# Kernel tuning notes

Measured on AMD Instinct MI355X. Metric: run time of the kernel, lower is better.

## Reference

```python
import jax, jax.numpy as jnp
import numpy as np

ROUTING_ITERS = 3

def squash(t, axis=-1):
    norm = jnp.linalg.norm(t, axis=axis, keepdims=True)
    scale = norm ** 2 / (1 + norm ** 2)
    return scale * t / (norm + 1e-08)

def setup_inputs() -> dict:
    key = jax.random.key(0)
    k1, k2 = jax.random.split(key)
    B, R, C, Din, Dout = 64, 4608, 32, 16, 16
    x = jax.random.normal(k1, (B, R, Din), dtype=jnp.float32)
    route_weights = jax.random.normal(k2, (R, C, Din, Dout), dtype=jnp.float32)
    return {"x": x, "route_weights": route_weights}

def reference(x, route_weights):
    # x: [B, R, Din], route_weights: [R, C, Din, Dout]
    B, R, _ = x.shape
    C = route_weights.shape[1]
    # u_hat: [B, R, C, Dout]  (prediction vectors)
    u_hat = jnp.einsum('bri,rcio->brco', x, route_weights)
    b_ij = jnp.zeros((B, R, C, 1), dtype=u_hat.dtype)
    v_j = None
    for _ in range(ROUTING_ITERS):
        c_ij = jax.nn.softmax(b_ij, axis=2)                    # coupling coeffs over capsules
        s_j = jnp.sum(c_ij * u_hat, axis=1, keepdims=True)     # [B, 1, C, Dout]
        v_j = squash(s_j, axis=-1)                             # [B, 1, C, Dout]
        b_ij = b_ij + jnp.sum(u_hat * v_j, axis=-1, keepdims=True)
    return v_j[:, 0]                                           # [B, C, Dout]
```

## Files before the change

### kernel.cpp

```cpp
#include <hip/hip_runtime.h>
#include <math.h>


#define B_    64
#define R_    4608
#define C_    32
#define RB    36
#define NBLK  (R_ / RB)
#define SELEM 32768

typedef _Float16 half8  __attribute__((ext_vector_type(8)));
typedef _Float16 half2v __attribute__((ext_vector_type(2)));
typedef float    f32x16 __attribute__((ext_vector_type(16)));

__device__ __forceinline__ void gload_lds16(const void* g, void* l) {
    __builtin_amdgcn_global_load_lds(
        (const __attribute__((address_space(1))) void*)g,
        (__attribute__((address_space(3))) void*)l, 16, 0, 0);
}

__global__ __launch_bounds__(512)
void caps_prep(const float* __restrict__ x, _Float16* __restrict__ xa)
{
    __shared__ _Float16 tl[8][64][16];
    const int t  = threadIdx.x;
    const int r0 = blockIdx.x * 8;

    {
        const int b = t >> 3, j8 = t & 7;
        const float4* xs = (const float4*)(x + ((size_t)b * R_ + r0 + j8) * 16);
        const float4 A = xs[0], Bv = xs[1], Cv = xs[2], Dv = xs[3];
        half8 lo, hi;
        lo[0]=(_Float16)A.x;  lo[1]=(_Float16)A.y;  lo[2]=(_Float16)A.z;  lo[3]=(_Float16)A.w;
        lo[4]=(_Float16)Bv.x; lo[5]=(_Float16)Bv.y; lo[6]=(_Float16)Bv.z; lo[7]=(_Float16)Bv.w;
        hi[0]=(_Float16)Cv.x; hi[1]=(_Float16)Cv.y; hi[2]=(_Float16)Cv.z; hi[3]=(_Float16)Cv.w;
        hi[4]=(_Float16)Dv.x; hi[5]=(_Float16)Dv.y; hi[6]=(_Float16)Dv.z; hi[7]=(_Float16)Dv.w;
        *(half8*)&tl[j8][b][0] = lo;
        *(half8*)&tl[j8][b][8] = hi;
    }
    __syncthreads();
    {
        const int rl = t >> 6, q = t & 63;
        _Float16* dst = xa + (size_t)(r0 + rl) * 1024 + q * 16;
        *(half8*)dst       = *(const half8*)&tl[rl][q][0];
        *(half8*)(dst + 8) = *(const half8*)&tl[rl][q][8];
    }
}

template<bool FIRST>
__global__ __launch_bounds__(1024, 4)
void caps_mfma(const _Float16* __restrict__ xa, const float* __restrict__ Wg,
               _Float16* __restrict__ wp, const float* __restrict__ vsumT,
               float* __restrict__ sdst)
{
    __shared__ _Float16 xalds[RB * 512];
    __shared__ float t_lds[32][33];
    __shared__ float c_lds[32][33];

    const int D     = blockIdx.x;
    const int xcd   = D & 7;
    const int slot  = D >> 3;
    const int chunk = (slot >> 1) * 8 + xcd;
    const int bh    = slot & 1;

    const int tid  = threadIdx.x;
    const int lane = tid & 63;
    const int wv   = tid >> 6;
    const int h    = lane >> 5;
    const int l31  = lane & 31;
    const int r0   = chunk * RB;
    const int bg   = bh * 32 + l31;

    {
        const int slx = (lane << 4) ^ (((lane >> 3) & 7) << 4);
        for (int t = wv; t < RB; t += 16) {
            const char* src = (const char*)xa + (size_t)(r0 + t) * 2048 + bh * 1024 + slx;
            gload_lds16(src, (char*)xalds + t * 1024);
        }
    }

    f32x16 sacc, zf;
#pragma unroll
    for (int k = 0; k < 16; ++k) { sacc[k] = 0.f; zf[k] = 0.f; }

    half2v vh[8];
    if (!FIRST) {
#pragma unroll
        for (int e = 0; e < 16; ++e) {
            const int g = wv * 32 + (e & 3) + 8 * (e >> 2) + 4 * h;
            vh[e >> 1][e & 1] = (_Float16)vsumT[(size_t)g * 64 + bg];
        }
    }

    asm volatile("s_waitcnt vmcnt(0)" ::: "memory");
    __syncthreads();

    const int avoff = ((l31 << 5) + (h << 4)) ^ (((l31 >> 2) & 7) << 4);

    const int c_ = 2 * wv + (l31 >> 4);
    const int o_ = l31 & 15;
#define WGATHER(dst, r)                                                           \
    do {                                                                          \
        const float* ws_ = Wg + (((size_t)(r) * 32 + c_) * 16 + 8 * h) * 16 + o_; \
        _Pragma("unroll")                                                         \
        for (int e_ = 0; e_ < 8; ++e_) dst[e_] = (_Float16)ws_[e_ * 16];          \
    } while (0)

    const size_t wstride = 16 * 64 * 8;
    half8 bc;
    if (FIRST) {
        WGATHER(bc, r0);
    } else {
        bc = *(const half8*)(wp + (((size_t)r0 * 16 + wv) * 64 + lane) * 8);
    }

#pragma unroll 1
    for (int t = 0; t < RB; ++t) {
        const half8 av = *(const half8*)((const char*)xalds + t * 1024 + avoff);

        if (FIRST) {
            sacc = __builtin_amdgcn_mfma_f32_32x32x16_f16(bc, av, sacc, 0, 0, 0);
            if (bh == 0)
                *(half8*)(wp + (((size_t)(r0 + t) * 16 + wv) * 64 + lane) * 8) = bc;
            if (t + 1 < RB) WGATHER(bc, r0 + t + 1);
            continue;
        }

        f32x16 u = __builtin_amdgcn_mfma_f32_32x32x16_f16(bc, av, zf, 0, 0, 0);

        const int tn = (t < RB - 1) ? (t + 1) : t;
        bc = *(const half8*)(wp + ((size_t)(r0 + tn)) * wstride
                                + ((size_t)wv * 64 + lane) * 8);

        {
            float s0 = 0.f, s1 = 0.f;
#pragma unroll
            for (int e2 = 0; e2 < 4; ++e2) {
                s0 += u[2 * e2]         * (float)vh[e2][0];
                s0 += u[2 * e2 + 1]     * (float)vh[e2][1];
                s1 += u[8 + 2 * e2]     * (float)vh[4 + e2][0];
                s1 += u[8 + 2 * e2 + 1] * (float)vh[4 + e2][1];
            }
            s0 += __shfl_xor(s0, 32);
            s1 += __shfl_xor(s1, 32);
            if (h == 0) {
                t_lds[2 * wv    ][l31] = s0;
                t_lds[2 * wv + 1][l31] = s1;
            }
        }
        __syncthreads();

        if (tid < 512) {
            const int a_ = lane & 15;
            const int b2 = tid >> 4;
            const float tA = t_lds[2 * a_][b2];
            const float tB = t_lds[2 * a_ + 1][b2];
            float m = fmaxf(tA, tB);
            m = fmaxf(m, __shfl_xor(m, 1));
            m = fmaxf(m, __shfl_xor(m, 2));
            m = fmaxf(m, __shfl_xor(m, 4));
            m = fmaxf(m, __shfl_xor(m, 8));
            const float eA = __expf(tA - m);
            const float eB = __expf(tB - m);
            float zs = eA + eB;
            zs += __shfl_xor(zs, 1);
            zs += __shfl_xor(zs, 2);
            zs += __shfl_xor(zs, 4);
            zs += __shfl_xor(zs, 8);
            const float inv = 1.0f / zs;
            c_lds[2 * a_][b2]     = eA * inv;
            c_lds[2 * a_ + 1][b2] = eB * inv;
        }
        __syncthreads();

        {
            const float c0v = c_lds[2 * wv    ][l31];
            const float c1v = c_lds[2 * wv + 1][l31];
#pragma unroll
            for (int e = 0; e < 8; ++e)  sacc[e] += c0v * u[e];
#pragma unroll
            for (int e = 8; e < 16; ++e) sacc[e] += c1v * u[e];
        }
    }
#undef WGATHER

    const float scale = FIRST ? 0.03125f : 1.0f;
    float* sp = sdst + ((size_t)chunk << 15);
#pragma unroll
    for (int e = 0; e < 16; ++e) {
        const int g = wv * 32 + (e & 3) + 8 * (e >> 2) + 4 * h;
        sp[(size_t)g * 64 + bg] = sacc[e] * scale;
    }
}

__global__ __launch_bounds__(256)
void caps_reduce1(const float* __restrict__ sp, float* __restrict__ s2)
{
    const int e  = blockIdx.x * 256 + threadIdx.x;
    const int pg = blockIdx.y;
    const float* p0 = sp + (size_t)pg * 16 * SELEM + e;
    float a = 0.0f;
#pragma unroll 8
    for (int p = 0; p < 16; ++p) a += p0[(size_t)p * SELEM];
    s2[pg * SELEM + e] = a;
}

__global__ __launch_bounds__(64)
void caps_reduce2T(const float* __restrict__ src, float* __restrict__ vsumT,
                   float* __restrict__ out, int mode)
{
    const int c = blockIdx.x;
    const int b = threadIdx.x;
    float a[16];
#pragma unroll
    for (int o = 0; o < 16; ++o) a[o] = 0.0f;
    for (int p = 0; p < 8; ++p)
#pragma unroll
        for (int o = 0; o < 16; ++o)
            a[o] += src[(size_t)p * SELEM + c * 1024 + o * 64 + b];
    float sq = 0.0f;
#pragma unroll
    for (int o = 0; o < 16; ++o) sq += a[o] * a[o];
    const float n  = sqrtf(sq);
    const float sc = sq / (1.0f + sq) / (n + 1e-8f);
    if (mode == 2) {
#pragma unroll
        for (int o = 0; o < 16; ++o)
            out[(size_t)b * 512 + c * 16 + o] = a[o] * sc;
    } else if (mode == 0) {
#pragma unroll
        for (int o = 0; o < 16; ++o)
            vsumT[c * 1024 + o * 64 + b] = a[o] * sc;
    } else {
#pragma unroll
        for (int o = 0; o < 16; ++o)
            vsumT[c * 1024 + o * 64 + b] += a[o] * sc;
    }
}

__global__ __launch_bounds__(256)
void caps_reduce2(const float* __restrict__ src, int P,
                  float* __restrict__ vsum, float* __restrict__ out, int mode)
{
    const int e = blockIdx.x * 256 + threadIdx.x;
    float a = 0.0f;
    for (int p = 0; p < P; ++p) a += src[(size_t)p * SELEM + e];
    float sq = a * a;
#pragma unroll
    for (int off = 8; off >= 1; off >>= 1) sq += __shfl_xor(sq, off);
    const float n = sqrtf(sq);
    const float v = a * (sq / (1.0f + sq) / (n + 1e-8f));
    if (mode == 0)      vsum[e] = v;
    else if (mode == 1) vsum[e] += v;
    else                out[e] = v;
}

template<bool FIRST>
__global__ __launch_bounds__(1024, 4)
void caps_pass_f32(const float* __restrict__ x, const float* __restrict__ W,
                   const float* __restrict__ vsumg, float* __restrict__ sdst)
{
    __shared__ float wlds[2][8192];
    const int tid = threadIdx.x, lane = tid & 63;
    const int c = tid & 31, dh = (tid >> 5) & 1, w = tid >> 6;
    const int r0 = blockIdx.x * RB, b0 = w << 2;
    const int key = (c & 7) << 4;
    const int cb  = (c << 10) + (dh << 5);

    float sacc[4][8];
#pragma unroll
    for (int q = 0; q < 4; ++q)
#pragma unroll
        for (int k = 0; k < 8; ++k) sacc[q][k] = 0.0f;

    float vreg[4][8];
    if (!FIRST) {
#pragma unroll
        for (int q = 0; q < 4; ++q) {
            const float4* vp = (const float4*)(vsumg + ((((b0+q) << 5) + c) << 4) + (dh << 3));
            float4 a = vp[0], bq = vp[1];
            vreg[q][0]=a.x; vreg[q][1]=a.y; vreg[q][2]=a.z; vreg[q][3]=a.w;
            vreg[q][4]=bq.x; vreg[q][5]=bq.y; vreg[q][6]=bq.z; vreg[q][7]=bq.w;
        }
    }

    const int Dloc0 = (w << 11);
    const int lx0 = (lane << 4) ^ ((((w << 1))     & 7) << 4);
    const int lx1 = (lane << 4) ^ ((((w << 1) | 1) & 7) << 4);
    const int wu = __builtin_amdgcn_readfirstlane(w);
    const float* xw = x + (size_t)((wu << 2) * R_ + r0) * 16;

#define STAGE(buf, r)                                                              \
    do {                                                                           \
        const char* wr_ = (const char*)W + ((size_t)(r) << 15);                    \
        gload_lds16(wr_ + Dloc0        + lx0, (char*)wlds[buf] + Dloc0);           \
        gload_lds16(wr_ + Dloc0 + 1024 + lx1, (char*)wlds[buf] + Dloc0 + 1024);    \
    } while (0)

    STAGE(0, r0);
#pragma unroll 1
    for (int t = 0; t < RB; ++t) {
        const int cur = t & 1;
        if (t + 1 < RB) { STAGE(cur ^ 1, r0 + t + 1); asm volatile("s_waitcnt vmcnt(2)" ::: "memory"); }
        else            { asm volatile("s_waitcnt vmcnt(0)" ::: "memory"); }
        __builtin_amdgcn_s_barrier();
        __builtin_amdgcn_sched_barrier(0);

        const char* lb = (const char*)wlds[cur];
        float u[4][8];
#pragma unroll
        for (int q = 0; q < 4; ++q)
#pragma unroll
            for (int k = 0; k < 8; ++k) u[q][k] = 0.0f;

#pragma unroll
        for (int i = 0; i < 16; ++i) {
            const int A = (cb + (i << 6)) ^ key;
            float4 w0 = *(const float4*)(lb + A);
            float4 w1 = *(const float4*)(lb + (A ^ 16));
            float wv[8] = {w0.x, w0.y, w0.z, w0.w, w1.x, w1.y, w1.z, w1.w};
#pragma unroll
            for (int q = 0; q < 4; ++q) {
                const float xv = xw[(size_t)q * (R_ * 16) + t * 16 + i];
#pragma unroll
                for (int k = 0; k < 8; ++k) u[q][k] = fmaf(xv, wv[k], u[q][k]);
            }
        }

#pragma unroll
        for (int q = 0; q < 4; ++q) {
            float cij;
            if (FIRST) cij = 0.03125f;
            else {
                float th = 0.0f;
#pragma unroll
                for (int k = 0; k < 8; ++k) th = fmaf(u[q][k], vreg[q][k], th);
                th += __shfl_xor(th, 32);
                float m = th;
#pragma unroll
                for (int off = 16; off >= 1; off >>= 1) m = fmaxf(m, __shfl_xor(m, off));
                const float e = __expf(th - m);
                float ssum = e;
#pragma unroll
                for (int off = 16; off >= 1; off >>= 1) ssum += __shfl_xor(ssum, off);
                cij = e / ssum;
            }
#pragma unroll
            for (int k = 0; k < 8; ++k) sacc[q][k] = fmaf(cij, u[q][k], sacc[q][k]);
        }
        __builtin_amdgcn_s_barrier();
    }
#undef STAGE

#pragma unroll
    for (int q = 0; q < 4; ++q) {
        float* sp = sdst + ((((b0+q) << 5) + c) << 4) + (dh << 3);
#pragma unroll
        for (int k = 0; k < 8; ++k) atomicAdd(sp + k, sacc[q][k]);
    }
}

extern "C" void kernel_launch(void* const* d_in, const int* in_sizes, int n_in,
                              void* d_out, int out_size, void* d_ws, size_t ws_size,
                              hipStream_t stream)
{
    const float* x = (const float*)d_in[0];
    const float* W = (const float*)d_in[1];
    float* out = (float*)d_out;

    const size_t WPB = (size_t)R_ * 16 * 64 * 8 * sizeof(_Float16);
    const size_t XAB = (size_t)R_ * 64 * 16 * sizeof(_Float16);
    const size_t SPB = (size_t)NBLK * SELEM * sizeof(float);
    const size_t S2B = (size_t)8 * SELEM * sizeof(float);
    const size_t VSB = (size_t)SELEM * sizeof(float);
    char* wsc = (char*)d_ws;

    if (ws_size >= WPB + XAB + SPB + S2B + VSB) {
        _Float16* wp  = (_Float16*)wsc;
        _Float16* xa  = (_Float16*)(wsc + WPB);
        float* s_part = (float*)(wsc + WPB + XAB);
        float* s2     = (float*)(wsc + WPB + XAB + SPB);
        float* vsumT  = (float*)(wsc + WPB + XAB + SPB + S2B);

        caps_prep<<<576, 512, 0, stream>>>(x, xa);

        caps_mfma<true ><<<256, 1024, 0, stream>>>(xa, W, wp, nullptr, s_part);
        caps_reduce1<<<dim3(128, 8), 256, 0, stream>>>(s_part, s2);
        caps_reduce2T<<<32, 64, 0, stream>>>(s2, vsumT, nullptr, 0);

        caps_mfma<false><<<256, 1024, 0, stream>>>(xa, W, wp, vsumT, s_part);
        caps_reduce1<<<dim3(128, 8), 256, 0, stream>>>(s_part, s2);
        caps_reduce2T<<<32, 64, 0, stream>>>(s2, vsumT, nullptr, 1);

        caps_mfma<false><<<256, 1024, 0, stream>>>(xa, W, wp, vsumT, s_part);
        caps_reduce1<<<dim3(128, 8), 256, 0, stream>>>(s_part, s2);
        caps_reduce2T<<<32, 64, 0, stream>>>(s2, vsumT, out, 2);
    } else {
        float* s    = (float*)wsc;
        float* vsum = s + SELEM;

        hipMemsetAsync(s, 0, VSB, stream);
        caps_pass_f32<true><<<NBLK, 1024, 0, stream>>>(x, W, nullptr, s);
        caps_reduce2<<<128, 256, 0, stream>>>(s, 1, vsum, nullptr, 0);

        hipMemsetAsync(s, 0, VSB, stream);
        caps_pass_f32<false><<<NBLK, 1024, 0, stream>>>(x, W, vsum, s);
        caps_reduce2<<<128, 256, 0, stream>>>(s, 1, vsum, nullptr, 1);

        hipMemsetAsync(s, 0, VSB, stream);
        caps_pass_f32<false><<<NBLK, 1024, 0, stream>>>(x, W, vsum, s);
        caps_reduce2<<<128, 256, 0, stream>>>(s, 1, nullptr, out, 2);
    }
}
```

Measured before the change: 156.3 us.

## Process two routing rows per iteration to halve barriers in routing loop

The non-first routing pass now handles two r rows per loop iteration: two MFMAs, two logit dot products, and a single pair of __syncthreads around a softmax that uses all 1024 threads (one row per half-block). The separate t/c LDS buffers are merged into one double-indexed buffer that is reused in place for the coefficients. This halves the number of block-wide barriers and raises occupancy of the softmax step, at the cost of more live registers (two u accumulators and two prefetched weight fragments). RB=36 is even, so the pairing is exact.

```diff
diff --git a/kernel.cpp b/kernel.cpp
--- a/kernel.cpp
+++ b/kernel.cpp
@@ -54,8 +54,7 @@
                float* __restrict__ sdst)
 {
     __shared__ _Float16 xalds[RB * 512];
-    __shared__ float t_lds[32][33];
-    __shared__ float c_lds[32][33];
+    __shared__ float tc_lds[2][32][33];
 
     const int D     = blockIdx.x;
     const int xcd   = D & 7;
@@ -107,79 +106,98 @@
     } while (0)
 
     const size_t wstride = 16 * 64 * 8;
-    half8 bc;
+
     if (FIRST) {
+        half8 bc;
         WGATHER(bc, r0);
-    } else {
-        bc = *(const half8*)(wp + (((size_t)r0 * 16 + wv) * 64 + lane) * 8);
-    }
-
 #pragma unroll 1
-    for (int t = 0; t < RB; ++t) {
-        const half8 av = *(const half8*)((const char*)xalds + t * 1024 + avoff);
-
-        if (FIRST) {
+        for (int t = 0; t < RB; ++t) {
+            const half8 av = *(const half8*)((const char*)xalds + t * 1024 + avoff);
             sacc = __builtin_amdgcn_mfma_f32_32x32x16_f16(bc, av, sacc, 0, 0, 0);
             if (bh == 0)
                 *(half8*)(wp + (((size_t)(r0 + t) * 16 + wv) * 64 + lane) * 8) = bc;
             if (t + 1 < RB) WGATHER(bc, r0 + t + 1);
-            continue;
-        }
-
-        f32x16 u = __builtin_amdgcn_mfma_f32_32x32x16_f16(bc, av, zf, 0, 0, 0);
-
-        const int tn = (t < RB - 1) ? (t + 1) : t;
-        bc = *(const half8*)(wp + ((size_t)(r0 + tn)) * wstride
-                                + ((size_t)wv * 64 + lane) * 8);
-
-        {
-            float s0 = 0.f, s1 = 0.f;
-#pragma unroll
-            for (int e2 = 0; e2 < 4; ++e2) {
-                s0 += u[2 * e2]         * (float)vh[e2][0];
-                s0 += u[2 * e2 + 1]     * (float)vh[e2][1];
-                s1 += u[8 + 2 * e2]     * (float)vh[4 + e2][0];
-                s1 += u[8 + 2 * e2 + 1] * (float)vh[4 + e2][1];
+        }
+    } else {
+        const _Float16* wpb = wp + ((size_t)wv * 64 + lane) * 8;
+        half8 bc0 = *(const half8*)(wpb + (size_t)(r0    ) * wstride);
+        half8 bc1 = *(const half8*)(wpb + (size_t)(r0 + 1) * wstride);
+
+#pragma unroll 1
+        for (int t = 0; t < RB; t += 2) {
+            const half8 av0 = *(const half8*)((const char*)xalds + (t    ) * 1024 + avoff);
+            const half8 av1 = *(const half8*)((const char*)xalds + (t + 1) * 1024 + avoff);
+
+            const f32x16 u0 = __builtin_amdgcn_mfma_f32_32x32x16_f16(bc0, av0, zf, 0, 0, 0);
+            const f32x16 u1 = __builtin_amdgcn_mfma_f32_32x32x16_f16(bc1, av1, zf, 0, 0, 0);
+
+            const int tn = (t + 2 < RB) ? (t + 2) : t;
+            bc0 = *(const half8*)(wpb + (size_t)(r0 + tn    ) * wstride);
+            bc1 = *(const half8*)(wpb + (size_t)(r0 + tn + 1) * wstride);
+
+            {
+                float a0 = 0.f, a1 = 0.f, b0 = 0.f, b1 = 0.f;
+#pragma unroll
+                for (int e2 = 0; e2 < 4; ++e2) {
+                    a0 += u0[2 * e2]         * (float)vh[e2][0];
+                    a0 += u0[2 * e2 + 1]     * (float)vh[e2][1];
+                    a1 += u0[8 + 2 * e2]     * (float)vh[4 + e2][0];
+                    a1 += u0[8 + 2 * e2 + 1] * (float)vh[4 + e2][1];
+                    b0 += u1[2 * e2]         * (float)vh[e2][0];
+                    b0 += u1[2 * e2 + 1]     * (float)vh[e2][1];
+                    b1 += u1[8 + 2 * e2]     * (float)vh[4 + e2][0];
+                    b1 += u1[8 + 2 * e2 + 1] * (float)vh[4 + e2][1];
+                }
+                a0 += __shfl_xor(a0, 32);
+                a1 += __shfl_xor(a1, 32);
+                b0 += __shfl_xor(b0, 32);
+                b1 += __shfl_xor(b1, 32);
+                if (h == 0) {
+                    tc_lds[0][2 * wv    ][l31] = a0;
+                    tc_lds[0][2 * wv + 1][l31] = a1;
+                    tc_lds[1][2 * wv    ][l31] = b0;
+                    tc_lds[1][2 * wv + 1][l31] = b1;
+                }
             }
-            s0 += __shfl_xor(s0, 32);
-            s1 += __shfl_xor(s1, 32);
-            if (h == 0) {
-                t_lds[2 * wv    ][l31] = s0;
-                t_lds[2 * wv + 1][l31] = s1;
+            __syncthreads();
+
+            {
+                const int rr   = tid >> 9;
+                const int tid5 = tid & 511;
+                const int a_   = tid5 & 15;
+                const int b2   = tid5 >> 4;
+                const float tA = tc_lds[rr][2 * a_][b2];
+                const float tB = tc_lds[rr][2 * a_ + 1][b2];
+                float m = fmaxf(tA, tB);
+                m = fmaxf(m, __shfl_xor(m, 1));
+                m = fmaxf(m, __shfl_xor(m, 2));
+                m = fmaxf(m, __shfl_xor(m, 4));
+                m = fmaxf(m, __shfl_xor(m, 8));
+                const float eA = __expf(tA - m);
+                const float eB = __expf(tB - m);
+                float zs = eA + eB;
+                zs += __shfl_xor(zs, 1);
+                zs += __shfl_xor(zs, 2);
+                zs += __shfl_xor(zs, 4);
+                zs += __shfl_xor(zs, 8);
+                const float inv = 1.0f / zs;
+                tc_lds[rr][2 * a_][b2]     = eA * inv;
+                tc_lds[rr][2 * a_ + 1][b2] = eB * inv;
             }
-        }
-        __syncthreads();
-
-        if (tid < 512) {
-            const int a_ = lane & 15;
-            const int b2 = tid >> 4;
-            const float tA = t_lds[2 * a_][b2];
-            const float tB = t_lds[2 * a_ + 1][b2];
-            float m = fmaxf(tA, tB);
-            m = fmaxf(m, __shfl_xor(m, 1));
-            m = fmaxf(m, __shfl_xor(m, 2));
-            m = fmaxf(m, __shfl_xor(m, 4));
-            m = fmaxf(m, __shfl_xor(m, 8));
-            const float eA = __expf(tA - m);
-            const float eB = __expf(tB - m);
-            float zs = eA + eB;
-            zs += __shfl_xor(zs, 1);
-            zs += __shfl_xor(zs, 2);
-            zs += __shfl_xor(zs, 4);
-            zs += __shfl_xor(zs, 8);
-            const float inv = 1.0f / zs;
-            c_lds[2 * a_][b2]     = eA * inv;
-            c_lds[2 * a_ + 1][b2] = eB * inv;
-        }
-        __syncthreads();
-
-        {
-            const float c0v = c_lds[2 * wv    ][l31];
-            const float c1v = c_lds[2 * wv + 1][l31];
-#pragma unroll
-            for (int e = 0; e < 8; ++e)  sacc[e] += c0v * u[e];
-#pragma unroll
-            for (int e = 8; e < 16; ++e) sacc[e] += c1v * u[e];
+            __syncthreads();
+
+            {
+                const float c00 = tc_lds[0][2 * wv    ][l31];
+                const float c01 = tc_lds[0][2 * wv + 1][l31];
+                const float c10 = tc_lds[1][2 * wv    ][l31];
+                const float c11 = tc_lds[1][2 * wv + 1][l31];
+#pragma unroll
+                for (int e = 0; e < 8; ++e)
+                    sacc[e] += c00 * u0[e] + c10 * u1[e];
+#pragma unroll
+                for (int e = 8; e < 16; ++e)
+                    sacc[e] += c01 * u0[e] + c11 * u1[e];
+            }
         }
     }
 #undef WGATHER
```

New measurement: 139.6 us. -10.7%, faster.
